# Kernel tuning notes

Hardware: AMD Instinct MI355X
Metric: run time of the kernel (lower is better)

## Reference

```python
import jax, jax.numpy as jnp
import numpy as np

H = 1024      # hidden_dim
F = 4 * H     # expert FFN dim
E = 16        # num_experts
K = 4         # num_experts_per_token


def setup_inputs() -> dict:
    key = jax.random.key(0)
    ks = jax.random.split(key, 10)
    s = 0.02
    return {
        "x": jax.random.normal(ks[0], (2, 1024, H), dtype=jnp.float32),
        # router: Linear(H,H) -> ReLU -> Linear(H,E)
        "Wr1": jax.random.normal(ks[1], (H, H), dtype=jnp.float32) * s,
        "br1": jnp.zeros((H,), dtype=jnp.float32),
        "Wr2": jax.random.normal(ks[2], (H, E), dtype=jnp.float32) * s,
        "br2": jnp.zeros((E,), dtype=jnp.float32),
        # stacked experts: Linear(H,4H) -> GELU -> Linear(4H,H)
        "W1": jax.random.normal(ks[3], (E, H, F), dtype=jnp.float32) * s,
        "b1": jnp.zeros((E, F), dtype=jnp.float32),
        "W2": jax.random.normal(ks[4], (E, F, H), dtype=jnp.float32) * s,
        "b2": jnp.zeros((E, H), dtype=jnp.float32),
    }


def reference(x, Wr1, br1, Wr2, br2, W1, b1, W2, b2):
    B, S, Hd = x.shape
    xf = x.reshape(-1, Hd)                       # [T, H]
    T = xf.shape[0]
    # router logits
    logits = jnp.maximum(xf @ Wr1 + br1, 0.0) @ Wr2 + br2   # [T, E]
    # top-k routing: softmax over the k selected logits
    topw, topi = jax.lax.top_k(logits, K)                    # [T, K]
    topw = jax.nn.softmax(topw, axis=-1)
    # dense combine weights c[t, e] = sum_k topw[t,k] * 1[topi[t,k]==e]
    c = jnp.zeros((T, E), dtype=xf.dtype)
    c = c.at[jnp.arange(T)[:, None], topi].add(topw)         # [T, E]
    # all-experts dense MLP (exact GELU, matching nn.GELU default)
    h = jax.nn.gelu(jnp.einsum('th,ehf->etf', xf, W1) + b1[:, None, :],
                    approximate=False)                       # [E, T, F]
    y = jnp.einsum('etf,efh->eth', h, W2) + b2[:, None, :]   # [E, T, H]
    out = jnp.einsum('eth,te->th', y, c)                     # [T, H]
    return out.reshape(B, S, Hd)
```

## Files before the change

### kernel.cpp

```cpp
#include <hip/hip_runtime.h>
#include <hip/hip_bf16.h>

#define T_TOK 2048
#define H_DIM 1024
#define F_DIM 4096
#define E_NUM 16
#define K_TOP 4

typedef float    floatx4 __attribute__((ext_vector_type(4)));
typedef _Float16 f16x8   __attribute__((ext_vector_type(8)));
typedef _Float16 f16x4   __attribute__((ext_vector_type(4)));

#define MiB (1024ull * 1024ull)
#define LOGIT_OFF ((size_t)0)
#define OFFS_OFF  (256ull * 1024)
#define TOKS_OFF  (320ull * 1024)
#define WSL_OFF   (384ull * 1024)
#define STK_OFF   (448ull * 1024)
#define TILEE_OFF (512ull * 1024)
#define TILEM_OFF (TILEE_OFF + 512)
#define TILEC_OFF (TILEM_OFF + 512)
#define XH_OFF    (1ull * MiB)
#define HBUF_OFF  (8ull * MiB)
#define YBUF_OFF  (72ull * MiB)
#define W1T_OFF   (104ull * MiB)
#define W2T_OFF   (232ull * MiB)
#define WS_NEED_FAST (360ull * MiB)

__device__ __forceinline__ void gload16(const void* g, void* l) {
  __builtin_amdgcn_global_load_lds(
      (const __attribute__((address_space(1))) unsigned int*)g,
      (__attribute__((address_space(3))) unsigned int*)l, 16, 0, 0);
}

__device__ __forceinline__ float gelu_fast(float v) {
  float z = 0.7978845608028654f * (v + 0.044715f * v * v * v);
  float e = __expf(2.f * z);
  float t = 1.f - 2.f / (e + 1.f);
  return 0.5f * v * (1.f + t);
}

__device__ __forceinline__ void cast_x_body(int blk, const float* __restrict__ x,
                                            _Float16* __restrict__ xh) {
  int i = blk * 256 + threadIdx.x;
  const floatx4* xin = reinterpret_cast<const floatx4*>(x) + (size_t)i * 2;
  floatx4 a = xin[0], b = xin[1];
  f16x8 o;
  o[0] = (_Float16)a[0]; o[1] = (_Float16)a[1]; o[2] = (_Float16)a[2]; o[3] = (_Float16)a[3];
  o[4] = (_Float16)b[0]; o[5] = (_Float16)b[1]; o[6] = (_Float16)b[2]; o[7] = (_Float16)b[3];
  *reinterpret_cast<f16x8*>(xh + (size_t)i * 8) = o;
}

__device__ __forceinline__ void tcast_body(const float* __restrict__ W,
                                           _Float16* __restrict__ Wt, int K, int N,
                                           int e, int k0, int n0, char* smem) {
  float (*Tt)[68] = (float(*)[68])smem;
  const float* We = W + (size_t)e * K * N;
  int t = threadIdx.x;
  int kk = t >> 4, nn = (t & 15) * 4;
#pragma unroll
  for (int j = 0; j < 4; j++) {
    int k = kk + 16 * j;
    floatx4 v = *reinterpret_cast<const floatx4*>(We + (size_t)(k0 + k) * N + n0 + nn);
    *reinterpret_cast<floatx4*>(&Tt[k][nn]) = v;
  }
  __syncthreads();
  int nr = t >> 2, kc = t & 3;
  f16x8 o0, o1;
#pragma unroll
  for (int j = 0; j < 8; j++) {
    o0[j] = (_Float16)Tt[kc * 16 + j][nr];
    o1[j] = (_Float16)Tt[kc * 16 + 8 + j][nr];
  }
  _Float16* dst = Wt + (size_t)e * N * K + (size_t)(n0 + nr) * K + k0 + kc * 16;
  *reinterpret_cast<f16x8*>(dst) = o0;
  *reinterpret_cast<f16x8*>(dst + 8) = o1;
}

__device__ __forceinline__ void router_gemm1_body(
    int m0, int n0, const float* __restrict__ x, const float* __restrict__ Wr1,
    const float* __restrict__ br1, float* __restrict__ hrf, char* smem) {
  _Float16 (*Ah)[40] = (_Float16(*)[40])(smem);
  _Float16 (*Al)[40] = (_Float16(*)[40])(smem + 5120);
  _Float16 (*Bh)[40] = (_Float16(*)[40])(smem + 10240);
  _Float16 (*Bl)[40] = (_Float16(*)[40])(smem + 15360);
  int tid = threadIdx.x;
  int arow = tid >> 2, achk = tid & 3;
  const float* Arow = x + (size_t)(m0 + arow) * H_DIM + achk * 8;
  int brow = tid >> 3, bq = tid & 7;

  floatx4 acc[2][2];
#pragma unroll
  for (int i = 0; i < 2; i++)
#pragma unroll
    for (int j = 0; j < 2; j++) acc[i][j] = (floatx4){0.f, 0.f, 0.f, 0.f};

  int wv = tid >> 6, lane = tid & 63;
  int wm = wv >> 1, wn = wv & 1;
  int lrow = lane & 15, lk = (lane >> 4) * 8;

  for (int k0 = 0; k0 < H_DIM; k0 += 32) {
    floatx4 a0 = *reinterpret_cast<const floatx4*>(Arow + k0);
    floatx4 a1 = *reinterpret_cast<const floatx4*>(Arow + k0 + 4);
    f16x8 hv, lv;
#pragma unroll
    for (int j = 0; j < 4; j++) {
      _Float16 hi = (_Float16)a0[j]; hv[j] = hi; lv[j] = (_Float16)(a0[j] - (float)hi);
      _Float16 hi2 = (_Float16)a1[j]; hv[4 + j] = hi2; lv[4 + j] = (_Float16)(a1[j] - (float)hi2);
    }
    *reinterpret_cast<f16x8*>(&Ah[arow][achk * 8]) = hv;
    *reinterpret_cast<f16x8*>(&Al[arow][achk * 8]) = lv;
    const float* wp = Wr1 + (size_t)(k0 + brow) * H_DIM + n0 + bq * 4;
    floatx4 w0 = *reinterpret_cast<const floatx4*>(wp);
    floatx4 w1 = *reinterpret_cast<const floatx4*>(wp + 32);
#pragma unroll
    for (int i = 0; i < 4; i++) {
      _Float16 h0 = (_Float16)w0[i];
      Bh[bq * 4 + i][brow] = h0; Bl[bq * 4 + i][brow] = (_Float16)(w0[i] - (float)h0);
      _Float16 h1 = (_Float16)w1[i];
      Bh[32 + bq * 4 + i][brow] = h1; Bl[32 + bq * 4 + i][brow] = (_Float16)(w1[i] - (float)h1);
    }
    __syncthreads();

    f16x8 ah0 = *reinterpret_cast<const f16x8*>(&Ah[32 * wm + lrow][lk]);
    f16x8 ah1 = *reinterpret_cast<const f16x8*>(&Ah[32 * wm + 16 + lrow][lk]);
    f16x8 al0 = *reinterpret_cast<const f16x8*>(&Al[32 * wm + lrow][lk]);
    f16x8 al1 = *reinterpret_cast<const f16x8*>(&Al[32 * wm + 16 + lrow][lk]);
    f16x8 bh0 = *reinterpret_cast<const f16x8*>(&Bh[32 * wn + lrow][lk]);
    f16x8 bh1 = *reinterpret_cast<const f16x8*>(&Bh[32 * wn + 16 + lrow][lk]);
    f16x8 bl0 = *reinterpret_cast<const f16x8*>(&Bl[32 * wn + lrow][lk]);
    f16x8 bl1 = *reinterpret_cast<const f16x8*>(&Bl[32 * wn + 16 + lrow][lk]);

    acc[0][0] = __builtin_amdgcn_mfma_f32_16x16x32_f16(ah0, bh0, acc[0][0], 0, 0, 0);
    acc[0][0] = __builtin_amdgcn_mfma_f32_16x16x32_f16(ah0, bl0, acc[0][0], 0, 0, 0);
    acc[0][0] = __builtin_amdgcn_mfma_f32_16x16x32_f16(al0, bh0, acc[0][0], 0, 0, 0);
    acc[0][1] = __builtin_amdgcn_mfma_f32_16x16x32_f16(ah0, bh1, acc[0][1], 0, 0, 0);
    acc[0][1] = __builtin_amdgcn_mfma_f32_16x16x32_f16(ah0, bl1, acc[0][1], 0, 0, 0);
    acc[0][1] = __builtin_amdgcn_mfma_f32_16x16x32_f16(al0, bh1, acc[0][1], 0, 0, 0);
    acc[1][0] = __builtin_amdgcn_mfma_f32_16x16x32_f16(ah1, bh0, acc[1][0], 0, 0, 0);
    acc[1][0] = __builtin_amdgcn_mfma_f32_16x16x32_f16(ah1, bl0, acc[1][0], 0, 0, 0);
    acc[1][0] = __builtin_amdgcn_mfma_f32_16x16x32_f16(al1, bh0, acc[1][0], 0, 0, 0);
    acc[1][1] = __builtin_amdgcn_mfma_f32_16x16x32_f16(ah1, bh1, acc[1][1], 0, 0, 0);
    acc[1][1] = __builtin_amdgcn_mfma_f32_16x16x32_f16(ah1, bl1, acc[1][1], 0, 0, 0);
    acc[1][1] = __builtin_amdgcn_mfma_f32_16x16x32_f16(al1, bh1, acc[1][1], 0, 0, 0);
    __syncthreads();
  }

#pragma unroll
  for (int am = 0; am < 2; am++) {
#pragma unroll
    for (int bn = 0; bn < 2; bn++) {
      int col = n0 + 32 * wn + 16 * bn + lrow;
      float bv = br1[col];
#pragma unroll
      for (int r = 0; r < 4; r++) {
        int rowt = 32 * wm + 16 * am + (lane >> 4) * 4 + r;
        float v = acc[am][bn][r] + bv;
        hrf[(size_t)(m0 + rowt) * H_DIM + col] = fmaxf(v, 0.f);
      }
    }
  }
}

#define P1_RG 512
#define P1_CX 1024
#define P1_T1 16384
#define P1_T2 16384
#define P1_TOTAL (P1_RG + P1_CX + P1_T1 + P1_T2)
__global__ __launch_bounds__(256) void fusedA_kernel(
    const float* __restrict__ x, const float* __restrict__ Wr1, const float* __restrict__ br1,
    float* __restrict__ hrf, const float* __restrict__ W1, _Float16* __restrict__ W1t,
    const float* __restrict__ W2, _Float16* __restrict__ W2t, _Float16* __restrict__ xh) {
  __shared__ __align__(16) char smem[20480];
  int bid = blockIdx.x;
  if (bid < P1_RG) {
    router_gemm1_body((bid >> 4) * 64, (bid & 15) * 64, x, Wr1, br1, hrf, smem);
  } else if (bid < P1_RG + P1_CX) {
    cast_x_body(bid - P1_RG, x, xh);
  } else if (bid < P1_RG + P1_CX + P1_T1) {
    int idx = bid - P1_RG - P1_CX;
    int nt = idx & 63, kt = (idx >> 6) & 15, e = idx >> 10;
    tcast_body(W1, W1t, H_DIM, F_DIM, e, kt * 64, nt * 64, smem);
  } else {
    int idx = bid - P1_RG - P1_CX - P1_T1;
    int nt = idx & 15, kt = (idx >> 4) & 63, e = idx >> 10;
    tcast_body(W2, W2t, F_DIM, H_DIM, e, kt * 64, nt * 64, smem);
  }
}

__global__ __launch_bounds__(256) void router_logits_kernel(
    const float* __restrict__ hrf, const float* __restrict__ Wr2,
    const float* __restrict__ br2, float* __restrict__ logits) {
  int t = blockIdx.x * 4 + (threadIdx.x >> 6);
  int lane = threadIdx.x & 63;
  float acc[E_NUM];
#pragma unroll
  for (int e = 0; e < E_NUM; e++) acc[e] = 0.f;
  const float* hr = hrf + (size_t)t * H_DIM;
#pragma unroll 4
  for (int i = 0; i < H_DIM / 64; i++) {
    int k = lane + 64 * i;
    float a = hr[k];
    const floatx4* w4 = reinterpret_cast<const floatx4*>(Wr2 + (size_t)k * E_NUM);
    floatx4 w0 = w4[0], w1 = w4[1], w2 = w4[2], w3 = w4[3];
#pragma unroll
    for (int j = 0; j < 4; j++) {
      acc[j]      += a * w0[j];
      acc[4 + j]  += a * w1[j];
      acc[8 + j]  += a * w2[j];
      acc[12 + j] += a * w3[j];
    }
  }
#pragma unroll
  for (int e = 0; e < E_NUM; e++) {
    float v = acc[e];
    for (int off = 32; off > 0; off >>= 1) v += __shfl_xor(v, off);
    if (lane == e) logits[(size_t)t * E_NUM + e] = v + br2[e];
  }
}

__global__ __launch_bounds__(1024) void routing_kernel(
    const float* __restrict__ logits, int* __restrict__ offs,
    int* __restrict__ toks, float* __restrict__ wsl, int* __restrict__ stk,
    int* __restrict__ tileE, int* __restrict__ tileM, int* __restrict__ tileC) {
  __shared__ int cnt[E_NUM], cur[E_NUM], loff[E_NUM + 1];
  int tid = threadIdx.x;
  if (tid < E_NUM) { cnt[tid] = 0; cur[tid] = 0; }
  __syncthreads();
  int ti[2][K_TOP]; float tw[2][K_TOP];
#pragma unroll
  for (int u = 0; u < 2; u++) {
    int t = u * 1024 + tid;
    float lg[E_NUM];
#pragma unroll
    for (int e = 0; e < E_NUM; e++) lg[e] = logits[(size_t)t * E_NUM + e];
    unsigned int used = 0;
    float vals[K_TOP];
#pragma unroll
    for (int k = 0; k < K_TOP; k++) {
      float best = -1e30f; int bi = 0;
#pragma unroll
      for (int e = 0; e < E_NUM; e++) {
        if (!((used >> e) & 1u) && lg[e] > best) { best = lg[e]; bi = e; }
      }
      used |= (1u << bi);
      vals[k] = best; ti[u][k] = bi;
    }
    float m = vals[0], s = 0.f;
#pragma unroll
    for (int k = 0; k < K_TOP; k++) { tw[u][k] = expf(vals[k] - m); s += tw[u][k]; }
    float inv = 1.f / s;
#pragma unroll
    for (int k = 0; k < K_TOP; k++) {
      tw[u][k] *= inv;
      atomicAdd(&cnt[ti[u][k]], 1);
    }
  }
  __syncthreads();
  if (tid == 0) {
    int acc = 0;
    loff[0] = 0; offs[0] = 0;
    for (int e = 0; e < E_NUM; e++) { acc += cnt[e]; loff[e + 1] = acc; offs[e + 1] = acc; }
    int idx = 0;
    for (int e = 0; e < E_NUM; e++) {
      for (int m0 = 0; m0 < cnt[e]; m0 += 128) { tileE[idx] = e; tileM[idx] = m0; idx++; }
    }
    tileC[0] = idx;
  }
  __syncthreads();
#pragma unroll
  for (int u = 0; u < 2; u++) {
    int t = u * 1024 + tid;
#pragma unroll
    for (int k = 0; k < K_TOP; k++) {
      int e = ti[u][k];
      int pos = atomicAdd(&cur[e], 1);
      int slot = loff[e] + pos;
      toks[slot] = t;
      wsl[slot] = tw[u][k];
      stk[t * K_TOP + k] = slot;
    }
  }
}

__global__ void combine_kernel(const _Float16* __restrict__ ybuf, const int* __restrict__ stk,
                               float* __restrict__ out) {
  int i = blockIdx.x * 256 + threadIdx.x;
  size_t p = (size_t)i * 8;
  int t = (int)(p >> 10);
  int h = (int)(p & 1023);
  float s[8] = {0.f, 0.f, 0.f, 0.f, 0.f, 0.f, 0.f, 0.f};
#pragma unroll
  for (int k = 0; k < K_TOP; k++) {
    int slot = stk[t * K_TOP + k];
    f16x8 v = *reinterpret_cast<const f16x8*>(ybuf + (size_t)slot * H_DIM + h);
#pragma unroll
    for (int j = 0; j < 8; j++) s[j] += (float)v[j];
  }
  floatx4 o0 = {s[0], s[1], s[2], s[3]};
  floatx4 o1 = {s[4], s[5], s[6], s[7]};
  *reinterpret_cast<floatx4*>(out + p) = o0;
  *reinterpret_cast<floatx4*>(out + p + 4) = o1;
}

template <int KK, int ACT, bool GATHER, bool SCALE>
__device__ __forceinline__ void moe_gemm_body(
    int ti, int n0, const _Float16* __restrict__ A, const _Float16* __restrict__ Bt,
    const float* __restrict__ bias, _Float16* __restrict__ Out,
    const int* __restrict__ offsets, const int* __restrict__ toklist,
    const float* __restrict__ wslot, const int* __restrict__ tileE,
    const int* __restrict__ tileM, const int* __restrict__ tileC,
    int N, char* smem) {
  if (ti >= tileC[0]) return;
  const int K = KK;
  int e = tileE[ti], m0 = tileM[ti];
  int base = offsets[e], cnt = offsets[e + 1] - base;

  _Float16 (*As)[128][32] = reinterpret_cast<_Float16(*)[128][32]>(smem);
  _Float16 (*Bs)[128][32] = reinterpret_cast<_Float16(*)[128][32]>(smem + 24576);

  int tid = threadIdx.x;
  int w = tid >> 6, lane = tid & 63;
  int wm = w >> 1, wn = w & 1;
  int lrow = lane & 15;

  int ar0 = w * 32 + (lane >> 2);
  int ar1 = ar0 + 16;
  int ach = (((lane & 3) ^ ((lane >> 3) & 3))) * 8;
  int mr0 = m0 + ar0; if (mr0 >= cnt) mr0 = cnt - 1;
  int mr1 = m0 + ar1; if (mr1 >= cnt) mr1 = cnt - 1;
  const _Float16* gA0 = A + (long)(GATHER ? toklist[base + mr0] : (base + mr0)) * K + ach;
  const _Float16* gA1 = A + (long)(GATHER ? toklist[base + mr1] : (base + mr1)) * K + ach;
  const _Float16* bge = Bt + (size_t)e * N * K;
  const _Float16* gB0 = bge + (long)(n0 + ar0) * K + ach;
  const _Float16* gB1 = bge + (long)(n0 + ar1) * K + ach;

  int phys8 = ((lane >> 4) ^ ((lrow >> 1) & 3)) * 8;

#define STAGE3(buf, kk) do { \
    gload16(gA0 + (kk), &As[buf][w * 32][0]); \
    gload16(gA1 + (kk), &As[buf][w * 32 + 16][0]); \
    gload16(gB0 + (kk), &Bs[buf][w * 32][0]); \
    gload16(gB1 + (kk), &Bs[buf][w * 32 + 16][0]); \
  } while (0)

#define COMPUTE3(buf) do { \
    f16x8 a[4], b[4]; \
    _Pragma("unroll") \
    for (int i = 0; i < 4; i++) { \
      a[i] = *reinterpret_cast<const f16x8*>(&As[buf][wm * 64 + i * 16 + lrow][phys8]); \
      b[i] = *reinterpret_cast<const f16x8*>(&Bs[buf][wn * 64 + i * 16 + lrow][phys8]); \
    } \
    __builtin_amdgcn_s_setprio(1); \
    _Pragma("unroll") \
    for (int i = 0; i < 4; i++) \
      _Pragma("unroll") \
      for (int j = 0; j < 4; j++) \
        acc[i][j] = __builtin_amdgcn_mfma_f32_16x16x32_f16(a[i], b[j], acc[i][j], 0, 0, 0); \
    __builtin_amdgcn_s_setprio(0); \
  } while (0)

  floatx4 acc[4][4];
#pragma unroll
  for (int i = 0; i < 4; i++)
#pragma unroll
    for (int j = 0; j < 4; j++) acc[i][j] = (floatx4){0.f, 0.f, 0.f, 0.f};

  constexpr int nk = KK / 32;
  STAGE3(0, 0);
  STAGE3(1, 32);

#pragma unroll 3
  for (int it = 0; it < nk - 1; ++it) {
    asm volatile("s_waitcnt vmcnt(4)" ::: "memory");
    __builtin_amdgcn_s_barrier();
    if (it + 2 < nk) STAGE3((it + 2) % 3, (it + 2) * 32);
    COMPUTE3(it % 3);
  }
  asm volatile("s_waitcnt vmcnt(0)" ::: "memory");
  __builtin_amdgcn_s_barrier();
  COMPUTE3((nk - 1) % 3);

#undef STAGE3
#undef COMPUTE3

  const float* be = bias + (size_t)e * N;
#pragma unroll
  for (int fm = 0; fm < 4; fm++) {
#pragma unroll
    for (int fn = 0; fn < 4; fn++) {
      int col = n0 + wn * 64 + fn * 16 + lrow;
      float bv = be[col];
#pragma unroll
      for (int r = 0; r < 4; r++) {
        int rowt = wm * 64 + fm * 16 + (lane >> 4) * 4 + r;
        int mg = m0 + rowt;
        if (mg < cnt) {
          float v = acc[fm][fn][r] + bv;
          if (ACT == 2) v = gelu_fast(v);
          long orow = base + mg;
          if (SCALE) v *= wslot[orow];
          Out[orow * (long)N + col] = (_Float16)v;
        }
      }
    }
  }
}

__global__ __launch_bounds__(256) void moe_gemm1_kernel(
    const _Float16* __restrict__ xh, const _Float16* __restrict__ W1t,
    const float* __restrict__ b1, _Float16* __restrict__ hbuf,
    const int* __restrict__ offsets, const int* __restrict__ toklist,
    const int* __restrict__ tileE, const int* __restrict__ tileM, const int* __restrict__ tileC) {
  __shared__ __align__(16) char smem[49152];
  moe_gemm_body<H_DIM, 2, true, false>(blockIdx.y, blockIdx.x * 128, xh, W1t, b1, hbuf,
                                       offsets, toklist, nullptr, tileE, tileM, tileC,
                                       F_DIM, smem);
}

__global__ __launch_bounds__(256) void moe_gemm2_kernel(
    const _Float16* __restrict__ hbuf, const _Float16* __restrict__ W2t,
    const float* __restrict__ b2, _Float16* __restrict__ ybuf,
    const int* __restrict__ offsets, const float* __restrict__ wslot,
    const int* __restrict__ tileE, const int* __restrict__ tileM, const int* __restrict__ tileC) {
  __shared__ __align__(16) char smem[49152];
  moe_gemm_body<F_DIM, 0, false, true>(blockIdx.y, blockIdx.x * 128, hbuf, W2t, b2, ybuf,
                                       offsets, nullptr, wslot, tileE, tileM, tileC,
                                       H_DIM, smem);
}

template <int ACT, bool GATHER, bool OFFS, bool SCALE>
__global__ __launch_bounds__(256) void moe_gemm(
    const _Float16* __restrict__ A, const float* __restrict__ W,
    const float* __restrict__ bias, _Float16* __restrict__ Out,
    const int* __restrict__ offsets, const int* __restrict__ toklist,
    const float* __restrict__ wslot, int M, int N, int K) {
  int e = blockIdx.z;
  int base = 0, cnt = M;
  if (OFFS) { base = offsets[e]; cnt = offsets[e + 1] - base; }
  int m0 = blockIdx.y * 64;
  if (m0 >= cnt) return;
  int n0 = blockIdx.x * 64;
  const float* We = W + (size_t)e * K * N;
  const float* be = bias + (size_t)e * N;

  __shared__ _Float16 As[64][40];
  __shared__ _Float16 Bs[64][40];

  int tid = threadIdx.x;
  int arow = tid >> 2, achk = tid & 3;
  int am_idx = m0 + arow; if (am_idx > cnt - 1) am_idx = cnt - 1;
  long arowg = GATHER ? (long)toklist[base + am_idx] : (long)(base + am_idx);
  const _Float16* Arow = A + arowg * (long)K + achk * 8;

  int brow = tid >> 3, bq = tid & 7;

  floatx4 acc[2][2];
#pragma unroll
  for (int i = 0; i < 2; i++)
#pragma unroll
    for (int j = 0; j < 2; j++) acc[i][j] = (floatx4){0.f, 0.f, 0.f, 0.f};

  int wv = tid >> 6, lane = tid & 63;
  int wm = wv >> 1, wn = wv & 1;
  int lrow = lane & 15, lk = (lane >> 4) * 8;

  for (int k0 = 0; k0 < K; k0 += 32) {
    *reinterpret_cast<f16x8*>(&As[arow][achk * 8]) = *reinterpret_cast<const f16x8*>(Arow + k0);
    const float* wp = We + (size_t)(k0 + brow) * N + n0 + bq * 4;
    floatx4 w0 = *reinterpret_cast<const floatx4*>(wp);
    floatx4 w1 = *reinterpret_cast<const floatx4*>(wp + 32);
#pragma unroll
    for (int i = 0; i < 4; i++) {
      Bs[bq * 4 + i][brow]      = (_Float16)w0[i];
      Bs[32 + bq * 4 + i][brow] = (_Float16)w1[i];
    }
    __syncthreads();

    f16x8 a0 = *reinterpret_cast<const f16x8*>(&As[32 * wm + lrow][lk]);
    f16x8 a1 = *reinterpret_cast<const f16x8*>(&As[32 * wm + 16 + lrow][lk]);
    f16x8 b0 = *reinterpret_cast<const f16x8*>(&Bs[32 * wn + lrow][lk]);
    f16x8 b1 = *reinterpret_cast<const f16x8*>(&Bs[32 * wn + 16 + lrow][lk]);
    acc[0][0] = __builtin_amdgcn_mfma_f32_16x16x32_f16(a0, b0, acc[0][0], 0, 0, 0);
    acc[0][1] = __builtin_amdgcn_mfma_f32_16x16x32_f16(a0, b1, acc[0][1], 0, 0, 0);
    acc[1][0] = __builtin_amdgcn_mfma_f32_16x16x32_f16(a1, b0, acc[1][0], 0, 0, 0);
    acc[1][1] = __builtin_amdgcn_mfma_f32_16x16x32_f16(a1, b1, acc[1][1], 0, 0, 0);
    __syncthreads();
  }

#pragma unroll
  for (int am = 0; am < 2; am++) {
#pragma unroll
    for (int bn = 0; bn < 2; bn++) {
      int col = n0 + 32 * wn + 16 * bn + lrow;
      float bv = be[col];
#pragma unroll
      for (int r = 0; r < 4; r++) {
        int rowt = 32 * wm + 16 * am + (lane >> 4) * 4 + r;
        int mg = m0 + rowt;
        if (mg < cnt) {
          float v = acc[am][bn][r] + bv;
          if (ACT == 2) v = gelu_fast(v);
          long orow = base + mg;
          if (SCALE) v *= wslot[orow];
          Out[orow * (long)N + col] = (_Float16)v;
        }
      }
    }
  }
}

__global__ void cast_x_kernel(const float* __restrict__ x, _Float16* __restrict__ xh) {
  cast_x_body(blockIdx.x, x, xh);
}

__global__ __launch_bounds__(256) void router_gemm1_kernel(
    const float* __restrict__ x, const float* __restrict__ Wr1,
    const float* __restrict__ br1, float* __restrict__ hrf) {
  __shared__ __align__(16) char smem[20480];
  router_gemm1_body(blockIdx.y * 64, blockIdx.x * 64, x, Wr1, br1, hrf, smem);
}

extern "C" void kernel_launch(void* const* d_in, const int* in_sizes, int n_in,
                              void* d_out, int out_size, void* d_ws, size_t ws_size,
                              hipStream_t stream) {
  const float* x   = (const float*)d_in[0];
  const float* Wr1 = (const float*)d_in[1];
  const float* br1 = (const float*)d_in[2];
  const float* Wr2 = (const float*)d_in[3];
  const float* br2 = (const float*)d_in[4];
  const float* W1  = (const float*)d_in[5];
  const float* b1  = (const float*)d_in[6];
  const float* W2  = (const float*)d_in[7];
  const float* b2  = (const float*)d_in[8];
  float* out = (float*)d_out;

  char* ws = (char*)d_ws;
  float* logits = (float*)(ws + LOGIT_OFF);
  int*   offs   = (int*)(ws + OFFS_OFF);
  int*   toks   = (int*)(ws + TOKS_OFF);
  float* wsl    = (float*)(ws + WSL_OFF);
  int*   stk    = (int*)(ws + STK_OFF);
  int*   tileE  = (int*)(ws + TILEE_OFF);
  int*   tileM  = (int*)(ws + TILEM_OFF);
  int*   tileC  = (int*)(ws + TILEC_OFF);
  _Float16* xh   = (_Float16*)(ws + XH_OFF);
  float*    hrf  = (float*)(ws + HBUF_OFF);
  _Float16* hbuf = (_Float16*)(ws + HBUF_OFF);
  _Float16* ybuf = (_Float16*)(ws + YBUF_OFF);
  _Float16* W1t  = (_Float16*)(ws + W1T_OFF);
  _Float16* W2t  = (_Float16*)(ws + W2T_OFF);

  bool fast = ws_size >= WS_NEED_FAST;

  if (fast) {
    fusedA_kernel<<<P1_TOTAL, 256, 0, stream>>>(x, Wr1, br1, hrf, W1, W1t, W2, W2t, xh);
  } else {
    cast_x_kernel<<<(T_TOK * H_DIM / 8) / 256, 256, 0, stream>>>(x, xh);
    router_gemm1_kernel<<<dim3(H_DIM / 64, T_TOK / 64), 256, 0, stream>>>(x, Wr1, br1, hrf);
  }

  router_logits_kernel<<<T_TOK / 4, 256, 0, stream>>>(hrf, Wr2, br2, logits);
  routing_kernel<<<1, 1024, 0, stream>>>(logits, offs, toks, wsl, stk, tileE, tileM, tileC);

  if (fast) {
    moe_gemm1_kernel<<<dim3(F_DIM / 128, 80), 256, 0, stream>>>(xh, W1t, b1, hbuf, offs, toks,
                                                                tileE, tileM, tileC);
    moe_gemm2_kernel<<<dim3(H_DIM / 128, 80), 256, 0, stream>>>(hbuf, W2t, b2, ybuf, offs, wsl,
                                                                tileE, tileM, tileC);
  } else {
    moe_gemm<2, true, true, false><<<dim3(F_DIM / 64, T_TOK / 64, E_NUM), 256, 0, stream>>>(
        xh, W1, b1, hbuf, offs, toks, nullptr, T_TOK, F_DIM, H_DIM);
    moe_gemm<0, false, true, true><<<dim3(H_DIM / 64, T_TOK / 64, E_NUM), 256, 0, stream>>>(
        hbuf, W2, b2, ybuf, offs, nullptr, wsl, T_TOK, H_DIM, F_DIM);
  }

  combine_kernel<<<(T_TOK * H_DIM / 8) / 256, 256, 0, stream>>>(ybuf, stk, out);
}
```

Baseline: 476.6 us.

## Reorder MoE GEMM tile grid, fix transpose bank conflicts, and reorder fused prologue blocks

```diff
diff --git a/kernel.cpp b/kernel.cpp
--- a/kernel.cpp
+++ b/kernel.cpp
@@ -54,7 +54,7 @@
 __device__ __forceinline__ void tcast_body(const float* __restrict__ W,
                                            _Float16* __restrict__ Wt, int K, int N,
                                            int e, int k0, int n0, char* smem) {
-  float (*Tt)[68] = (float(*)[68])smem;
+  float (*Tt)[69] = (float(*)[69])smem;
   const float* We = W + (size_t)e * K * N;
   int t = threadIdx.x;
   int kk = t >> 4, nn = (t & 15) * 4;
@@ -65,16 +65,16 @@
     *reinterpret_cast<floatx4*>(&Tt[k][nn]) = v;
   }
   __syncthreads();
-  int nr = t >> 2, kc = t & 3;
-  f16x8 o0, o1;
-#pragma unroll
-  for (int j = 0; j < 8; j++) {
-    o0[j] = (_Float16)Tt[kc * 16 + j][nr];
-    o1[j] = (_Float16)Tt[kc * 16 + 8 + j][nr];
-  }
-  _Float16* dst = Wt + (size_t)e * N * K + (size_t)(n0 + nr) * K + k0 + kc * 16;
-  *reinterpret_cast<f16x8*>(dst) = o0;
-  *reinterpret_cast<f16x8*>(dst + 8) = o1;
+  int nr = t >> 3, kc = t & 7;
+  _Float16* dste = Wt + (size_t)e * N * K;
+#pragma unroll
+  for (int half = 0; half < 2; half++) {
+    int n = nr + half * 32;
+    f16x8 o;
+#pragma unroll
+    for (int j = 0; j < 8; j++) o[j] = (_Float16)Tt[kc * 8 + j][n];
+    *reinterpret_cast<f16x8*>(dste + (size_t)(n0 + n) * K + k0 + kc * 8) = o;
+  }
 }
 
 __device__ __forceinline__ void router_gemm1_body(
@@ -162,29 +162,30 @@
   }
 }
 
+#define P1_T2 16384
 #define P1_RG 512
 #define P1_CX 1024
 #define P1_T1 16384
-#define P1_T2 16384
-#define P1_TOTAL (P1_RG + P1_CX + P1_T1 + P1_T2)
+#define P1_TOTAL (P1_T2 + P1_RG + P1_CX + P1_T1)
 __global__ __launch_bounds__(256) void fusedA_kernel(
     const float* __restrict__ x, const float* __restrict__ Wr1, const float* __restrict__ br1,
     float* __restrict__ hrf, const float* __restrict__ W1, _Float16* __restrict__ W1t,
     const float* __restrict__ W2, _Float16* __restrict__ W2t, _Float16* __restrict__ xh) {
   __shared__ __align__(16) char smem[20480];
   int bid = blockIdx.x;
-  if (bid < P1_RG) {
-    router_gemm1_body((bid >> 4) * 64, (bid & 15) * 64, x, Wr1, br1, hrf, smem);
-  } else if (bid < P1_RG + P1_CX) {
-    cast_x_body(bid - P1_RG, x, xh);
-  } else if (bid < P1_RG + P1_CX + P1_T1) {
-    int idx = bid - P1_RG - P1_CX;
+  if (bid < P1_T2) {
+    int idx = bid;
+    int nt = idx & 15, kt = (idx >> 4) & 63, e = idx >> 10;
+    tcast_body(W2, W2t, F_DIM, H_DIM, e, kt * 64, nt * 64, smem);
+  } else if (bid < P1_T2 + P1_RG) {
+    int g = bid - P1_T2;
+    router_gemm1_body((g >> 4) * 64, (g & 15) * 64, x, Wr1, br1, hrf, smem);
+  } else if (bid < P1_T2 + P1_RG + P1_CX) {
+    cast_x_body(bid - P1_T2 - P1_RG, x, xh);
+  } else {
+    int idx = bid - P1_T2 - P1_RG - P1_CX;
     int nt = idx & 63, kt = (idx >> 6) & 15, e = idx >> 10;
     tcast_body(W1, W1t, H_DIM, F_DIM, e, kt * 64, nt * 64, smem);
-  } else {
-    int idx = bid - P1_RG - P1_CX - P1_T1;
-    int nt = idx & 15, kt = (idx >> 4) & 63, e = idx >> 10;
-    tcast_body(W2, W2t, F_DIM, H_DIM, e, kt * 64, nt * 64, smem);
   }
 }
 
@@ -413,7 +414,9 @@
     const int* __restrict__ offsets, const int* __restrict__ toklist,
     const int* __restrict__ tileE, const int* __restrict__ tileM, const int* __restrict__ tileC) {
   __shared__ __align__(16) char smem[49152];
-  moe_gemm_body<H_DIM, 2, true, false>(blockIdx.y, blockIdx.x * 128, xh, W1t, b1, hbuf,
+  int x = blockIdx.x;
+  int ti = (x & 7) * 10 + (x >> 3);
+  moe_gemm_body<H_DIM, 2, true, false>(ti, blockIdx.y * 128, xh, W1t, b1, hbuf,
                                        offsets, toklist, nullptr, tileE, tileM, tileC,
                                        F_DIM, smem);
 }
@@ -424,7 +427,9 @@
     const int* __restrict__ offsets, const float* __restrict__ wslot,
     const int* __restrict__ tileE, const int* __restrict__ tileM, const int* __restrict__ tileC) {
   __shared__ __align__(16) char smem[49152];
-  moe_gemm_body<F_DIM, 0, false, true>(blockIdx.y, blockIdx.x * 128, hbuf, W2t, b2, ybuf,
+  int x = blockIdx.x;
+  int ti = (x & 7) * 10 + (x >> 3);
+  moe_gemm_body<F_DIM, 0, false, true>(ti, blockIdx.y * 128, hbuf, W2t, b2, ybuf,
                                        offsets, nullptr, wslot, tileE, tileM, tileC,
                                        H_DIM, smem);
 }
@@ -564,9 +569,9 @@
   routing_kernel<<<1, 1024, 0, stream>>>(logits, offs, toks, wsl, stk, tileE, tileM, tileC);
 
   if (fast) {
-    moe_gemm1_kernel<<<dim3(F_DIM / 128, 80), 256, 0, stream>>>(xh, W1t, b1, hbuf, offs, toks,
+    moe_gemm1_kernel<<<dim3(80, F_DIM / 128), 256, 0, stream>>>(xh, W1t, b1, hbuf, offs, toks,
                                                                 tileE, tileM, tileC);
-    moe_gemm2_kernel<<<dim3(H_DIM / 128, 80), 256, 0, stream>>>(hbuf, W2t, b2, ybuf, offs, wsl,
+    moe_gemm2_kernel<<<dim3(80, H_DIM / 128), 256, 0, stream>>>(hbuf, W2t, b2, ybuf, offs, wsl,
                                                                 tileE, tileM, tileC);
   } else {
     moe_gemm<2, true, true, false><<<dim3(F_DIM / 64, T_TOK / 64, E_NUM), 256, 0, stream>>>(
```

Measured after the change: 483.8 us. About the same (+1.5%).

## Read fp32 expert weights directly in MoE GEMMs, drop pre-transpose cast

Applied to the files above, without the earlier changes.

```diff
diff --git a/kernel.cpp b/kernel.cpp
--- a/kernel.cpp
+++ b/kernel.cpp
@@ -9,7 +9,7 @@
 
 typedef float    floatx4 __attribute__((ext_vector_type(4)));
 typedef _Float16 f16x8   __attribute__((ext_vector_type(8)));
-typedef _Float16 f16x4   __attribute__((ext_vector_type(4)));
+typedef __fp16   fp16v2  __attribute__((ext_vector_type(2)));
 
 #define MiB (1024ull * 1024ull)
 #define LOGIT_OFF ((size_t)0)
@@ -23,9 +23,7 @@
 #define XH_OFF    (1ull * MiB)
 #define HBUF_OFF  (8ull * MiB)
 #define YBUF_OFF  (72ull * MiB)
-#define W1T_OFF   (104ull * MiB)
-#define W2T_OFF   (232ull * MiB)
-#define WS_NEED_FAST (360ull * MiB)
+#define WS_NEED_FAST (96ull * MiB)
 
 __device__ __forceinline__ void gload16(const void* g, void* l) {
   __builtin_amdgcn_global_load_lds(
@@ -49,32 +47,6 @@
   o[0] = (_Float16)a[0]; o[1] = (_Float16)a[1]; o[2] = (_Float16)a[2]; o[3] = (_Float16)a[3];
   o[4] = (_Float16)b[0]; o[5] = (_Float16)b[1]; o[6] = (_Float16)b[2]; o[7] = (_Float16)b[3];
   *reinterpret_cast<f16x8*>(xh + (size_t)i * 8) = o;
-}
-
-__device__ __forceinline__ void tcast_body(const float* __restrict__ W,
-                                           _Float16* __restrict__ Wt, int K, int N,
-                                           int e, int k0, int n0, char* smem) {
-  float (*Tt)[68] = (float(*)[68])smem;
-  const float* We = W + (size_t)e * K * N;
-  int t = threadIdx.x;
-  int kk = t >> 4, nn = (t & 15) * 4;
-#pragma unroll
-  for (int j = 0; j < 4; j++) {
-    int k = kk + 16 * j;
-    floatx4 v = *reinterpret_cast<const floatx4*>(We + (size_t)(k0 + k) * N + n0 + nn);
-    *reinterpret_cast<floatx4*>(&Tt[k][nn]) = v;
-  }
-  __syncthreads();
-  int nr = t >> 2, kc = t & 3;
-  f16x8 o0, o1;
-#pragma unroll
-  for (int j = 0; j < 8; j++) {
-    o0[j] = (_Float16)Tt[kc * 16 + j][nr];
-    o1[j] = (_Float16)Tt[kc * 16 + 8 + j][nr];
-  }
-  _Float16* dst = Wt + (size_t)e * N * K + (size_t)(n0 + nr) * K + k0 + kc * 16;
-  *reinterpret_cast<f16x8*>(dst) = o0;
-  *reinterpret_cast<f16x8*>(dst + 8) = o1;
 }
 
 __device__ __forceinline__ void router_gemm1_body(
@@ -164,27 +136,16 @@
 
 #define P1_RG 512
 #define P1_CX 1024
-#define P1_T1 16384
-#define P1_T2 16384
-#define P1_TOTAL (P1_RG + P1_CX + P1_T1 + P1_T2)
+#define P1_TOTAL (P1_RG + P1_CX)
 __global__ __launch_bounds__(256) void fusedA_kernel(
     const float* __restrict__ x, const float* __restrict__ Wr1, const float* __restrict__ br1,
-    float* __restrict__ hrf, const float* __restrict__ W1, _Float16* __restrict__ W1t,
-    const float* __restrict__ W2, _Float16* __restrict__ W2t, _Float16* __restrict__ xh) {
+    float* __restrict__ hrf, _Float16* __restrict__ xh) {
   __shared__ __align__(16) char smem[20480];
   int bid = blockIdx.x;
   if (bid < P1_RG) {
     router_gemm1_body((bid >> 4) * 64, (bid & 15) * 64, x, Wr1, br1, hrf, smem);
-  } else if (bid < P1_RG + P1_CX) {
+  } else {
     cast_x_body(bid - P1_RG, x, xh);
-  } else if (bid < P1_RG + P1_CX + P1_T1) {
-    int idx = bid - P1_RG - P1_CX;
-    int nt = idx & 63, kt = (idx >> 6) & 15, e = idx >> 10;
-    tcast_body(W1, W1t, H_DIM, F_DIM, e, kt * 64, nt * 64, smem);
-  } else {
-    int idx = bid - P1_RG - P1_CX - P1_T1;
-    int nt = idx & 15, kt = (idx >> 4) & 63, e = idx >> 10;
-    tcast_body(W2, W2t, F_DIM, H_DIM, e, kt * 64, nt * 64, smem);
   }
 }
 
@@ -305,7 +266,7 @@
 
 template <int KK, int ACT, bool GATHER, bool SCALE>
 __device__ __forceinline__ void moe_gemm_body(
-    int ti, int n0, const _Float16* __restrict__ A, const _Float16* __restrict__ Bt,
+    int ti, int n0, const _Float16* __restrict__ A, const float* __restrict__ Bf,
     const float* __restrict__ bias, _Float16* __restrict__ Out,
     const int* __restrict__ offsets, const int* __restrict__ toklist,
     const float* __restrict__ wslot, const int* __restrict__ tileE,
@@ -317,12 +278,12 @@
   int base = offsets[e], cnt = offsets[e + 1] - base;
 
   _Float16 (*As)[128][32] = reinterpret_cast<_Float16(*)[128][32]>(smem);
-  _Float16 (*Bs)[128][32] = reinterpret_cast<_Float16(*)[128][32]>(smem + 24576);
+  float (*Bs)[32][128] = reinterpret_cast<float(*)[32][128]>(smem + 24576);
 
   int tid = threadIdx.x;
   int w = tid >> 6, lane = tid & 63;
   int wm = w >> 1, wn = w & 1;
-  int lrow = lane & 15;
+  int lrow = lane & 15, hi = lane >> 4;
 
   int ar0 = w * 32 + (lane >> 2);
   int ar1 = ar0 + 16;
@@ -331,25 +292,44 @@
   int mr1 = m0 + ar1; if (mr1 >= cnt) mr1 = cnt - 1;
   const _Float16* gA0 = A + (long)(GATHER ? toklist[base + mr0] : (base + mr0)) * K + ach;
   const _Float16* gA1 = A + (long)(GATHER ? toklist[base + mr1] : (base + mr1)) * K + ach;
-  const _Float16* bge = Bt + (size_t)e * N * K;
-  const _Float16* gB0 = bge + (long)(n0 + ar0) * K + ach;
-  const _Float16* gB1 = bge + (long)(n0 + ar1) * K + ach;
+  const float* Bfe = Bf + (size_t)e * (size_t)K * (size_t)N;
+  const float* gB = Bfe + (size_t)(8 * w + (lane >> 5)) * N + n0 +
+                    ((((lane & 31) ^ ((w & 1) << 2))) << 2);
 
   int phys8 = ((lane >> 4) ^ ((lrow >> 1) & 3)) * 8;
+  int bswz = (hi & 1) << 4;
 
 #define STAGE3(buf, kk) do { \
     gload16(gA0 + (kk), &As[buf][w * 32][0]); \
     gload16(gA1 + (kk), &As[buf][w * 32 + 16][0]); \
-    gload16(gB0 + (kk), &Bs[buf][w * 32][0]); \
-    gload16(gB1 + (kk), &Bs[buf][w * 32 + 16][0]); \
+    gload16(gB + (size_t)(kk) * N,         &Bs[buf][8 * w + 0][0]); \
+    gload16(gB + (size_t)(kk) * N + 2 * N, &Bs[buf][8 * w + 2][0]); \
+    gload16(gB + (size_t)(kk) * N + 4 * N, &Bs[buf][8 * w + 4][0]); \
+    gload16(gB + (size_t)(kk) * N + 6 * N, &Bs[buf][8 * w + 6][0]); \
   } while (0)
 
 #define COMPUTE3(buf) do { \
     f16x8 a[4], b[4]; \
     _Pragma("unroll") \
+    for (int i = 0; i < 4; i++) \
+      a[i] = *reinterpret_cast<const f16x8*>(&As[buf][wm * 64 + i * 16 + lrow][phys8]); \
+    _Pragma("unroll") \
     for (int i = 0; i < 4; i++) { \
-      a[i] = *reinterpret_cast<const f16x8*>(&As[buf][wm * 64 + i * 16 + lrow][phys8]); \
-      b[i] = *reinterpret_cast<const f16x8*>(&Bs[buf][wn * 64 + i * 16 + lrow][phys8]); \
+      int pcol = (wn * 64 + i * 16 + lrow) ^ bswz; \
+      float f0 = Bs[buf][hi * 8 + 0][pcol]; \
+      float f1 = Bs[buf][hi * 8 + 1][pcol]; \
+      float f2 = Bs[buf][hi * 8 + 2][pcol]; \
+      float f3 = Bs[buf][hi * 8 + 3][pcol]; \
+      float f4 = Bs[buf][hi * 8 + 4][pcol]; \
+      float f5 = Bs[buf][hi * 8 + 5][pcol]; \
+      float f6 = Bs[buf][hi * 8 + 6][pcol]; \
+      float f7 = Bs[buf][hi * 8 + 7][pcol]; \
+      union { fp16v2 h[4]; f16x8 v; } u; \
+      u.h[0] = __builtin_amdgcn_cvt_pkrtz(f0, f1); \
+      u.h[1] = __builtin_amdgcn_cvt_pkrtz(f2, f3); \
+      u.h[2] = __builtin_amdgcn_cvt_pkrtz(f4, f5); \
+      u.h[3] = __builtin_amdgcn_cvt_pkrtz(f6, f7); \
+      b[i] = u.v; \
     } \
     __builtin_amdgcn_s_setprio(1); \
     _Pragma("unroll") \
@@ -372,7 +352,7 @@
 
 #pragma unroll 3
   for (int it = 0; it < nk - 1; ++it) {
-    asm volatile("s_waitcnt vmcnt(4)" ::: "memory");
+    asm volatile("s_waitcnt vmcnt(6)" ::: "memory");
     __builtin_amdgcn_s_barrier();
     if (it + 2 < nk) STAGE3((it + 2) % 3, (it + 2) * 32);
     COMPUTE3(it % 3);
@@ -408,23 +388,27 @@
 }
 
 __global__ __launch_bounds__(256) void moe_gemm1_kernel(
-    const _Float16* __restrict__ xh, const _Float16* __restrict__ W1t,
+    const _Float16* __restrict__ xh, const float* __restrict__ W1,
     const float* __restrict__ b1, _Float16* __restrict__ hbuf,
     const int* __restrict__ offsets, const int* __restrict__ toklist,
     const int* __restrict__ tileE, const int* __restrict__ tileM, const int* __restrict__ tileC) {
-  __shared__ __align__(16) char smem[49152];
-  moe_gemm_body<H_DIM, 2, true, false>(blockIdx.y, blockIdx.x * 128, xh, W1t, b1, hbuf,
+  __shared__ __align__(16) char smem[73728];
+  int x = blockIdx.x;
+  int ti = (x & 7) * 10 + (x >> 3);
+  moe_gemm_body<H_DIM, 2, true, false>(ti, blockIdx.y * 128, xh, W1, b1, hbuf,
                                        offsets, toklist, nullptr, tileE, tileM, tileC,
                                        F_DIM, smem);
 }
 
 __global__ __launch_bounds__(256) void moe_gemm2_kernel(
-    const _Float16* __restrict__ hbuf, const _Float16* __restrict__ W2t,
+    const _Float16* __restrict__ hbuf, const float* __restrict__ W2,
     const float* __restrict__ b2, _Float16* __restrict__ ybuf,
     const int* __restrict__ offsets, const float* __restrict__ wslot,
     const int* __restrict__ tileE, const int* __restrict__ tileM, const int* __restrict__ tileC) {
-  __shared__ __align__(16) char smem[49152];
-  moe_gemm_body<F_DIM, 0, false, true>(blockIdx.y, blockIdx.x * 128, hbuf, W2t, b2, ybuf,
+  __shared__ __align__(16) char smem[73728];
+  int x = blockIdx.x;
+  int ti = (x & 7) * 10 + (x >> 3);
+  moe_gemm_body<F_DIM, 0, false, true>(ti, blockIdx.y * 128, hbuf, W2, b2, ybuf,
                                        offsets, nullptr, wslot, tileE, tileM, tileC,
                                        H_DIM, smem);
 }
@@ -548,13 +532,11 @@
   float*    hrf  = (float*)(ws + HBUF_OFF);
   _Float16* hbuf = (_Float16*)(ws + HBUF_OFF);
   _Float16* ybuf = (_Float16*)(ws + YBUF_OFF);
-  _Float16* W1t  = (_Float16*)(ws + W1T_OFF);
-  _Float16* W2t  = (_Float16*)(ws + W2T_OFF);
 
   bool fast = ws_size >= WS_NEED_FAST;
 
   if (fast) {
-    fusedA_kernel<<<P1_TOTAL, 256, 0, stream>>>(x, Wr1, br1, hrf, W1, W1t, W2, W2t, xh);
+    fusedA_kernel<<<P1_TOTAL, 256, 0, stream>>>(x, Wr1, br1, hrf, xh);
   } else {
     cast_x_kernel<<<(T_TOK * H_DIM / 8) / 256, 256, 0, stream>>>(x, xh);
     router_gemm1_kernel<<<dim3(H_DIM / 64, T_TOK / 64), 256, 0, stream>>>(x, Wr1, br1, hrf);
@@ -564,9 +546,9 @@
   routing_kernel<<<1, 1024, 0, stream>>>(logits, offs, toks, wsl, stk, tileE, tileM, tileC);
 
   if (fast) {
-    moe_gemm1_kernel<<<dim3(F_DIM / 128, 80), 256, 0, stream>>>(xh, W1t, b1, hbuf, offs, toks,
+    moe_gemm1_kernel<<<dim3(80, F_DIM / 128), 256, 0, stream>>>(xh, W1, b1, hbuf, offs, toks,
                                                                 tileE, tileM, tileC);
-    moe_gemm2_kernel<<<dim3(H_DIM / 128, 80), 256, 0, stream>>>(hbuf, W2t, b2, ybuf, offs, wsl,
+    moe_gemm2_kernel<<<dim3(80, H_DIM / 128), 256, 0, stream>>>(hbuf, W2, b2, ybuf, offs, wsl,
                                                                 tileE, tileM, tileC);
   } else {
     moe_gemm<2, true, true, false><<<dim3(F_DIM / 64, T_TOK / 64, E_NUM), 256, 0, stream>>>(
```

After: 485.9 us. No clear change (+2.0%).
